# Performance work log

Hardware: AMD Instinct MI355X
Metric: run time of the kernel (lower is better)

Reference implementation:

```python
import jax, jax.numpy as jnp
import numpy as np

D_MODEL = 512
N_HEADS = 8
D_K = 64
B, T = 64, 256


def setup_inputs() -> dict:
    key = jax.random.key(0)
    ks = jax.random.split(key, 5)
    x = jax.random.normal(ks[0], (B, T, D_MODEL), dtype=jnp.float32)
    s = 1.0 / np.sqrt(D_MODEL)
    Wq = jax.random.normal(ks[1], (N_HEADS, D_MODEL, D_K), dtype=jnp.float32) * s
    Wk = jax.random.normal(ks[2], (N_HEADS, D_MODEL, D_K), dtype=jnp.float32) * s
    Wv = jax.random.normal(ks[3], (N_HEADS, D_MODEL, D_K), dtype=jnp.float32) * s
    Wo = jax.random.normal(ks[4], (N_HEADS * D_K, D_MODEL), dtype=jnp.float32) * s
    return {"x": x, "Wq": Wq, "Wk": Wk, "Wv": Wv, "Wo": Wo}


def reference(x, Wq, Wk, Wv, Wo):
    Bc, Tc, C = x.shape  # C == d_model; source scales by C**0.5, not sqrt(d_k)
    q = jnp.einsum('btc,hcd->bhtd', x, Wq)
    k = jnp.einsum('btc,hcd->bhtd', x, Wk)
    v = jnp.einsum('btc,hcd->bhtd', x, Wv)
    scores = jnp.einsum('bhtd,bhsd->bhts', q, k) / jnp.sqrt(jnp.float32(C))
    causal = jnp.tril(jnp.ones((Tc, Tc), dtype=bool))
    scores = jnp.where(causal, scores, -jnp.inf)
    attn = jax.nn.softmax(scores, axis=-1)  # dropout = identity in eval mode
    out = jnp.einsum('bhts,bhsd->bhtd', attn, v)
    out = out.transpose(0, 2, 1, 3).reshape(Bc, Tc, -1)  # concat heads
    return out @ Wo  # final dropout = identity in eval mode
```

## Files before the change

kernel.cpp:

```cpp
#include <hip/hip_runtime.h>
#include <hip/hip_bf16.h>

typedef __attribute__((ext_vector_type(4))) float f32x4;
typedef __attribute__((ext_vector_type(8))) short bf16x8;
typedef __attribute__((ext_vector_type(4))) short s16x4;
typedef __attribute__((ext_vector_type(4))) unsigned int u32x4;

#define DEV static __device__ __forceinline__

DEV unsigned short f2b(float f) {
  union { float f; unsigned int u; } v; v.f = f;
  unsigned int u = v.u;
  return (unsigned short)((u + 0x7fffu + ((u >> 16) & 1u)) >> 16);
}

DEV void gll16(const void* g, void* l) {
  __builtin_amdgcn_global_load_lds((__attribute__((address_space(1))) void*)g,
                                   (__attribute__((address_space(3))) void*)l,
                                   16, 0, 0);
}

__global__ __launch_bounds__(256) void prep(const float* __restrict__ x,
                                            const float* __restrict__ Wq,
                                            const float* __restrict__ Wk,
                                            const float* __restrict__ Wv,
                                            const float* __restrict__ Wo,
                                            unsigned short* __restrict__ xb,
                                            unsigned short* __restrict__ Wt,
                                            unsigned short* __restrict__ WoT) {
  const int bid = blockIdx.x;
  if (bid < 8192) {
    int id = bid * 256 + threadIdx.x;
    f32x4 v = *(const f32x4*)(x + (long)id * 4);
    s16x4 o;
    o.x = (short)f2b(v.x); o.y = (short)f2b(v.y);
    o.z = (short)f2b(v.z); o.w = (short)f2b(v.w);
    *(s16x4*)(xb + (long)id * 4) = o;
    return;
  }

  __shared__ unsigned int L[64 * 65];
  const int tx = threadIdx.x & 63;
  const int ty = threadIdx.x >> 6;

  int tb = bid - 8192;
  if (tb < 192) {
    int proj = tb >> 6, h = (tb >> 3) & 7, c0 = (tb & 7) << 6;
    const float* W = (proj == 0) ? Wq : ((proj == 1) ? Wk : Wv);
    const float* base = W + (long)h * 32768 + (long)c0 * 64;
#pragma unroll
    for (int i = 0; i < 16; i++) {
      int c = ty + i * 4;
      L[tx * 65 + c] = f2b(base[(long)c * 64 + tx]);
    }
    __syncthreads();
    unsigned short* out = Wt + ((long)(proj * 512 + h * 64)) * 512 + c0;
#pragma unroll
    for (int i = 0; i < 16; i++) {
      int d = ty + i * 4;
      out[(long)d * 512 + tx] = (unsigned short)L[d * 65 + tx];
    }
  } else {
    int t = tb - 192;
    int n0 = (t >> 3) << 6, c0 = (t & 7) << 6;
#pragma unroll
    for (int i = 0; i < 16; i++) {
      int c = ty + i * 4;
      L[tx * 65 + c] = f2b(Wo[(long)(c0 + c) * 512 + n0 + tx]);
    }
    __syncthreads();
    unsigned short* out = WoT + (long)n0 * 512 + c0;
#pragma unroll
    for (int i = 0; i < 16; i++) {
      int n = ty + i * 4;
      out[(long)n * 512 + tx] = (unsigned short)L[n * 65 + tx];
    }
  }
}

template <int F32OUT>
__global__ __launch_bounds__(256, 3) void gemm_bt(const unsigned short* __restrict__ A,
                                                  const unsigned short* __restrict__ BT,
                                                  void* __restrict__ Cv,
                                                  int N) {
  const int K = 512;
  __shared__ unsigned short As[3][128 * 32];
  __shared__ unsigned short Bs[3][128 * 32];

  const int tid = threadIdx.x;
  const int wave = tid >> 6, lane = tid & 63;
  const int quad = lane >> 4, l16 = lane & 15;
  const int wm = wave >> 1, wn = wave & 1;

  const int NB = N >> 7;
  const int nwg = gridDim.x;
  const int q = nwg >> 3, r = nwg & 7;
  const int xcd = blockIdx.x & 7, ci = blockIdx.x >> 3;
  const int wg = (xcd < r ? xcd * (q + 1) : r * (q + 1) + (xcd - r) * q) + ci;
  const int bn = wg % NB;
  const int bm = wg / NB;

  const int srow = lane >> 2;
  const int scg = lane & 3;

  f32x4 acc[4][4] = {};

  auto stage = [&](int t, int buf) {
#pragma unroll
    for (int i = 0; i < 2; i++) {
      int seg = wave * 2 + i;
      int rr = seg * 16 + srow;
      int gc = (scg ^ ((rr >> 1) & 3)) * 8;
      gll16(A + (long)(bm * 128 + rr) * K + t * 32 + gc, &As[buf][seg * 512]);
      gll16(BT + (long)(bn * 128 + rr) * K + t * 32 + gc, &Bs[buf][seg * 512]);
    }
  };

  auto compute = [&](int buf) {
    bf16x8 af[4], bfv[4];
#pragma unroll
    for (int mt = 0; mt < 4; mt++) {
      int rr = wm * 64 + mt * 16 + l16;
      af[mt] = *(const bf16x8*)(&As[buf][rr * 32 + ((quad ^ ((rr >> 1) & 3)) * 8)]);
    }
#pragma unroll
    for (int nt = 0; nt < 4; nt++) {
      int rr = wn * 64 + nt * 16 + l16;
      bfv[nt] = *(const bf16x8*)(&Bs[buf][rr * 32 + ((quad ^ ((rr >> 1) & 3)) * 8)]);
    }
#pragma unroll
    for (int mt = 0; mt < 4; mt++)
#pragma unroll
      for (int nt = 0; nt < 4; nt++)
        acc[mt][nt] = __builtin_amdgcn_mfma_f32_16x16x32_bf16(af[mt], bfv[nt], acc[mt][nt], 0, 0, 0);
  };

  stage(0, 0);
  stage(1, 1);

#pragma unroll
  for (int t = 0; t < 16; t++) {
    if (t + 2 < 16) stage(t + 2, (t + 2) % 3);
    if (t < 14)       asm volatile("s_waitcnt vmcnt(8)" ::: "memory");
    else if (t == 14) asm volatile("s_waitcnt vmcnt(4)" ::: "memory");
    else              asm volatile("s_waitcnt vmcnt(0)" ::: "memory");
    __builtin_amdgcn_s_barrier();
    __builtin_amdgcn_sched_barrier(0);
    compute(t % 3);
    __builtin_amdgcn_sched_barrier(0);
    __builtin_amdgcn_s_barrier();
  }

#pragma unroll
  for (int mt = 0; mt < 4; mt++) {
#pragma unroll
    for (int nt = 0; nt < 4; nt++) {
      int row0 = bm * 128 + wm * 64 + mt * 16 + quad * 4;
      int col = bn * 128 + wn * 64 + nt * 16 + l16;
      if (F32OUT) {
        float* cp = (float*)Cv + (long)row0 * N + col;
#pragma unroll
        for (int r2 = 0; r2 < 4; r2++)
          cp[(long)r2 * N] = acc[mt][nt][r2];
      } else {
        unsigned short* cp = (unsigned short*)Cv + (long)row0 * N + col;
#pragma unroll
        for (int r2 = 0; r2 < 4; r2++)
          cp[(long)r2 * N] = f2b(acc[mt][nt][r2]);
      }
    }
  }
}

__global__ __launch_bounds__(256, 2) void attn(const unsigned short* __restrict__ QKV,
                                               unsigned short* __restrict__ AO) {
  const int bh = blockIdx.x;
  const int b = bh >> 3, h = bh & 7;
  const int tid = threadIdx.x;
  const int wave = tid >> 6, lane = tid & 63;
  const int quad = lane >> 4, l16 = lane & 15;

  __shared__ unsigned short Kl[256 * 64];
  __shared__ unsigned short Vt[64 * 264];
  __shared__ unsigned short Pl[4][32 * 40];

  const unsigned short* Qb = QKV + (long)b * 256 * 1536 + h * 64;
  const unsigned short* Kb = Qb + 512;
  const unsigned short* Vb = Qb + 1024;

  {
    int r = lane >> 3, cg = lane & 7;
#pragma unroll
    for (int s = 0; s < 8; s++) {
      int seg = wave * 8 + s;
      gll16(Kb + (long)(seg * 8 + r) * 1536 + ((cg ^ r) * 8), Kl + seg * 512);
    }
  }
  {
    int j = tid;
    const unsigned short* vp = Vb + (long)j * 1536;
#pragma unroll
    for (int g = 0; g < 8; g++) {
      union { u32x4 v; unsigned short s[8]; } d;
      d.v = *(const u32x4*)(vp + g * 8);
#pragma unroll
      for (int q = 0; q < 8; q++)
        Vt[(g * 8 + q) * 264 + j] = d.s[q];
    }
  }
  const int tiles[2] = {wave, 7 - wave};
  bf16x8 qf[2][2][2];
#pragma unroll
  for (int ti = 0; ti < 2; ti++)
#pragma unroll
    for (int kc = 0; kc < 2; kc++)
#pragma unroll
      for (int mt = 0; mt < 2; mt++)
        qf[ti][kc][mt] = *(const bf16x8*)(Qb +
            (long)(tiles[ti] * 32 + mt * 16 + l16) * 1536 + kc * 32 + quad * 8);

  __syncthreads();

  f32x4 O[2][2][4] = {};
  float lsum[2][2][4] = {};
  const float scale = 0.044194173824159216f;

#pragma unroll
  for (int ti = 0; ti < 2; ti++) {
    const int t = tiles[ti];
    for (int c32 = 0; c32 <= t; c32++) {
      f32x4 S[2][2] = {};
#pragma unroll
      for (int kc = 0; kc < 2; kc++) {
        bf16x8 kbf[2];
#pragma unroll
        for (int st = 0; st < 2; st++) {
          int jrow = c32 * 32 + st * 16 + l16;
          kbf[st] = *(const bf16x8*)(Kl + jrow * 64 + (((kc * 4 + quad) ^ (jrow & 7)) * 8));
        }
#pragma unroll
        for (int mt = 0; mt < 2; mt++)
#pragma unroll
          for (int st = 0; st < 2; st++)
            S[mt][st] = __builtin_amdgcn_mfma_f32_16x16x32_bf16(qf[ti][kc][mt], kbf[st], S[mt][st], 0, 0, 0);
      }
      const bool diag = (c32 == t);
#pragma unroll
      for (int mt = 0; mt < 2; mt++)
#pragma unroll
        for (int st = 0; st < 2; st++)
#pragma unroll
          for (int r = 0; r < 4; r++) {
            int trow = mt * 16 + quad * 4 + r;
            float p = __expf(S[mt][st][r] * scale);
            if (diag && (st * 16 + l16 > trow)) p = 0.0f;
            lsum[ti][mt][r] += p;
            Pl[wave][trow * 40 + st * 16 + l16] = f2b(p);
          }
      bf16x8 pa[2], vbf[4];
#pragma unroll
      for (int mt = 0; mt < 2; mt++)
        pa[mt] = *(const bf16x8*)(&Pl[wave][(mt * 16 + l16) * 40 + quad * 8]);
#pragma unroll
      for (int dt = 0; dt < 4; dt++)
        vbf[dt] = *(const bf16x8*)(Vt + (dt * 16 + l16) * 264 + c32 * 32 + quad * 8);
#pragma unroll
      for (int mt = 0; mt < 2; mt++)
#pragma unroll
        for (int dt = 0; dt < 4; dt++)
          O[ti][mt][dt] = __builtin_amdgcn_mfma_f32_16x16x32_bf16(pa[mt], vbf[dt], O[ti][mt][dt], 0, 0, 0);
    }
  }

  float linv[2][2][4];
#pragma unroll
  for (int ti = 0; ti < 2; ti++)
#pragma unroll
    for (int mt = 0; mt < 2; mt++)
#pragma unroll
      for (int r = 0; r < 4; r++) {
        float s = lsum[ti][mt][r];
        s += __shfl_xor(s, 1); s += __shfl_xor(s, 2);
        s += __shfl_xor(s, 4); s += __shfl_xor(s, 8);
        linv[ti][mt][r] = 1.0f / s;
      }
#pragma unroll
  for (int ti = 0; ti < 2; ti++)
#pragma unroll
    for (int mt = 0; mt < 2; mt++)
#pragma unroll
      for (int dt = 0; dt < 4; dt++)
#pragma unroll
        for (int r = 0; r < 4; r++) {
          int t_ = tiles[ti] * 32 + mt * 16 + quad * 4 + r;
          int d = dt * 16 + l16;
          AO[(long)(b * 256 + t_) * 512 + h * 64 + d] = f2b(O[ti][mt][dt][r] * linv[ti][mt][r]);
        }
}

extern "C" void kernel_launch(void* const* d_in, const int* in_sizes, int n_in,
                              void* d_out, int out_size, void* d_ws, size_t ws_size,
                              hipStream_t stream) {
  const float* x  = (const float*)d_in[0];
  const float* Wq = (const float*)d_in[1];
  const float* Wk = (const float*)d_in[2];
  const float* Wv = (const float*)d_in[3];
  const float* Wo = (const float*)d_in[4];

  unsigned short* Wt  = (unsigned short*)d_ws;
  unsigned short* WoT = Wt + 1536 * 512;
  unsigned short* xb  = WoT + 512 * 512;
  unsigned short* QKV = xb + (long)16384 * 512;
  unsigned short* AO  = QKV + (long)16384 * 1536;
  float* out = (float*)d_out;

  prep<<<8448, 256, 0, stream>>>(x, Wq, Wk, Wv, Wo, xb, Wt, WoT);

  gemm_bt<0><<<1536, 256, 0, stream>>>(xb, Wt, (void*)QKV, 1536);

  attn<<<512, 256, 0, stream>>>(QKV, AO);

  gemm_bt<1><<<512, 256, 0, stream>>>(AO, WoT, (void*)out, 512);
}
```

Before: 161.9 us.

## Enlarge GEMM tiles to 128x256 with 8 waves, K=64 double-buffered pipeline

Rewrites the bf16 GEMM kernel to use 512-thread workgroups computing 128x256 output tiles, with K-step 64 and double-buffered LDS instead of a K=32 triple buffer. Global-to-LDS loads are interleaved between MFMA k-slices, and s_setprio raises wave priority during compute. The aim is more data reuse per LDS byte and fewer barriers per FLOP. In exchange, occupancy drops (64KB+ LDS, 2 blocks), and the grid shrinks to 768 and 256 blocks, which may underfill the CUs for the output projection.

```diff
diff --git a/kernel.cpp b/kernel.cpp
--- a/kernel.cpp
+++ b/kernel.cpp
@@ -79,20 +79,20 @@
 }
 
 template <int F32OUT>
-__global__ __launch_bounds__(256, 3) void gemm_bt(const unsigned short* __restrict__ A,
+__global__ __launch_bounds__(512, 2) void gemm_bt(const unsigned short* __restrict__ A,
                                                   const unsigned short* __restrict__ BT,
                                                   void* __restrict__ Cv,
                                                   int N) {
   const int K = 512;
-  __shared__ unsigned short As[3][128 * 32];
-  __shared__ unsigned short Bs[3][128 * 32];
+  __shared__ unsigned short Ash[2][128 * 64];
+  __shared__ unsigned short Bsh[2][256 * 64];
 
   const int tid = threadIdx.x;
   const int wave = tid >> 6, lane = tid & 63;
   const int quad = lane >> 4, l16 = lane & 15;
-  const int wm = wave >> 1, wn = wave & 1;
-
-  const int NB = N >> 7;
+  const int wm = wave >> 2, wn = wave & 3;
+
+  const int NB = N >> 8;
   const int nwg = gridDim.x;
   const int q = nwg >> 3, r = nwg & 7;
   const int xcd = blockIdx.x & 7, ci = blockIdx.x >> 3;
@@ -100,33 +100,34 @@
   const int bn = wg % NB;
   const int bm = wg / NB;
 
-  const int srow = lane >> 2;
-  const int scg = lane & 3;
+  const int r8 = lane >> 3, cg = lane & 7;
+  const int gc = (cg ^ r8) * 8;
+
+  const unsigned short* Abase = A + (long)(bm * 128 + wave * 8 + r8) * K + gc;
+  const unsigned short* Bbase = BT + (long)(bn * 256 + wave * 8 + r8) * K + gc;
 
   f32x4 acc[4][4] = {};
 
-  auto stage = [&](int t, int buf) {
-#pragma unroll
-    for (int i = 0; i < 2; i++) {
-      int seg = wave * 2 + i;
-      int rr = seg * 16 + srow;
-      int gc = (scg ^ ((rr >> 1) & 3)) * 8;
-      gll16(A + (long)(bm * 128 + rr) * K + t * 32 + gc, &As[buf][seg * 512]);
-      gll16(BT + (long)(bn * 128 + rr) * K + t * 32 + gc, &Bs[buf][seg * 512]);
-    }
+  auto stageA = [&](int kt, int buf, int issue) {
+    gll16(Abase + (long)issue * 64 * K + kt * 64,
+          &Ash[buf][(issue * 64 + wave * 8) * 64]);
   };
-
-  auto compute = [&](int buf) {
+  auto stageB = [&](int kt, int buf, int issue) {
+    gll16(Bbase + (long)issue * 64 * K + kt * 64,
+          &Bsh[buf][(issue * 64 + wave * 8) * 64]);
+  };
+
+  auto kslice = [&](int buf, int kc) {
     bf16x8 af[4], bfv[4];
 #pragma unroll
     for (int mt = 0; mt < 4; mt++) {
       int rr = wm * 64 + mt * 16 + l16;
-      af[mt] = *(const bf16x8*)(&As[buf][rr * 32 + ((quad ^ ((rr >> 1) & 3)) * 8)]);
+      af[mt] = *(const bf16x8*)(&Ash[buf][rr * 64 + (((kc * 4 + quad) ^ (rr & 7)) * 8)]);
     }
 #pragma unroll
     for (int nt = 0; nt < 4; nt++) {
-      int rr = wn * 64 + nt * 16 + l16;
-      bfv[nt] = *(const bf16x8*)(&Bs[buf][rr * 32 + ((quad ^ ((rr >> 1) & 3)) * 8)]);
+      int rb = wn * 64 + nt * 16 + l16;
+      bfv[nt] = *(const bf16x8*)(&Bsh[buf][rb * 64 + (((kc * 4 + quad) ^ (rb & 7)) * 8)]);
     }
 #pragma unroll
     for (int mt = 0; mt < 4; mt++)
@@ -135,20 +136,25 @@
         acc[mt][nt] = __builtin_amdgcn_mfma_f32_16x16x32_bf16(af[mt], bfv[nt], acc[mt][nt], 0, 0, 0);
   };
 
-  stage(0, 0);
-  stage(1, 1);
-
-#pragma unroll
-  for (int t = 0; t < 16; t++) {
-    if (t + 2 < 16) stage(t + 2, (t + 2) % 3);
-    if (t < 14)       asm volatile("s_waitcnt vmcnt(8)" ::: "memory");
-    else if (t == 14) asm volatile("s_waitcnt vmcnt(4)" ::: "memory");
-    else              asm volatile("s_waitcnt vmcnt(0)" ::: "memory");
+  stageB(0, 0, 0); stageB(0, 0, 1); stageB(0, 0, 2); stageB(0, 0, 3);
+  stageA(0, 0, 0); stageA(0, 0, 1);
+
+#pragma unroll
+  for (int kt = 0; kt < 8; kt++) {
+    const int bc = kt & 1, bs = bc ^ 1;
     __builtin_amdgcn_s_barrier();
     __builtin_amdgcn_sched_barrier(0);
-    compute(t % 3);
+    if (kt < 7) { stageB(kt + 1, bs, 0); stageB(kt + 1, bs, 1); }
+    if (kt < 7) asm volatile("s_waitcnt vmcnt(2)" ::: "memory");
+    else        asm volatile("s_waitcnt vmcnt(0)" ::: "memory");
+    __builtin_amdgcn_s_barrier();
     __builtin_amdgcn_sched_barrier(0);
-    __builtin_amdgcn_s_barrier();
+    __builtin_amdgcn_s_setprio(1);
+    kslice(bc, 0);
+    if (kt < 7) { stageB(kt + 1, bs, 2); stageB(kt + 1, bs, 3); }
+    kslice(bc, 1);
+    if (kt < 7) { stageA(kt + 1, bs, 0); stageA(kt + 1, bs, 1); }
+    __builtin_amdgcn_s_setprio(0);
   }
 
 #pragma unroll
@@ -156,7 +162,7 @@
 #pragma unroll
     for (int nt = 0; nt < 4; nt++) {
       int row0 = bm * 128 + wm * 64 + mt * 16 + quad * 4;
-      int col = bn * 128 + wn * 64 + nt * 16 + l16;
+      int col = bn * 256 + wn * 64 + nt * 16 + l16;
       if (F32OUT) {
         float* cp = (float*)Cv + (long)row0 * N + col;
 #pragma unroll
@@ -316,9 +322,9 @@
 
   prep<<<8448, 256, 0, stream>>>(x, Wq, Wk, Wv, Wo, xb, Wt, WoT);
 
-  gemm_bt<0><<<1536, 256, 0, stream>>>(xb, Wt, (void*)QKV, 1536);
+  gemm_bt<0><<<768, 512, 0, stream>>>(xb, Wt, (void*)QKV, 1536);
 
   attn<<<512, 256, 0, stream>>>(QKV, AO);
 
-  gemm_bt<1><<<512, 256, 0, stream>>>(AO, WoT, (void*)out, 512);
-}
+  gemm_bt<1><<<256, 512, 0, stream>>>(AO, WoT, (void*)out, 512);
+}
```

Result: no change. 162.6 us (+0.5%).
